# Performance work log

Hardware: AMD Instinct MI355X
Metric: run time of the kernel (lower is better)

## Reference

```python
import jax, jax.numpy as jnp
import numpy as np

WS = (4, 4, 4)          # window size (D, H, W)
DIM = 96
HEADS = 8
HEAD_DIM = DIM // HEADS
SCALE = HEAD_DIM ** (-0.5)
N = WS[0] * WS[1] * WS[2]  # 64 tokens per window


def _relative_position_index(ws):
    coords = np.stack(np.meshgrid(np.arange(ws[0]), np.arange(ws[1]), np.arange(ws[2]), indexing='ij'))
    cf = coords.reshape(3, -1)                       # [3, N]
    rel = cf[:, :, None] - cf[:, None, :]            # [3, N, N]
    rel = rel.transpose(1, 2, 0).astype(np.int64)    # [N, N, 3]
    rel[:, :, 0] += ws[0] - 1
    rel[:, :, 1] += ws[1] - 1
    rel[:, :, 2] += ws[2] - 1
    rel[:, :, 0] *= (2 * ws[1] - 1) * (2 * ws[2] - 1)
    rel[:, :, 1] *= 2 * ws[2] - 1
    return jnp.asarray(rel.sum(-1))                  # [N, N]

REL_IDX = _relative_position_index(WS)


def setup_inputs() -> dict:
    key = jax.random.key(0)
    ks = jax.random.split(key, 6)
    B = 4096   # total windows (64 images x 64 windows)
    nW = 64
    table_size = (2 * WS[0] - 1) * (2 * WS[1] - 1) * (2 * WS[2] - 1)  # 343
    return {
        'x': jax.random.normal(ks[0], (B, N, DIM), jnp.float32),
        'mask': jax.random.normal(ks[1], (nW, N, N), jnp.float32),
        'qkv_w': jax.random.normal(ks[2], (3 * DIM, DIM), jnp.float32) * 0.02,
        'proj_w': jax.random.normal(ks[3], (DIM, DIM), jnp.float32) * 0.02,
        'proj_b': jnp.zeros((DIM,), jnp.float32),
        'bias_table': jax.random.normal(ks[4], (table_size, HEADS), jnp.float32) * 0.02,
    }


def reference(x, mask, qkv_w, proj_w, proj_b, bias_table):
    B, n, C = x.shape
    # QKV projection (torch Linear: y = x @ W.T), split into heads
    qkv = (x @ qkv_w.T).reshape(B, n, 3, HEADS, HEAD_DIM)
    qkv = jnp.transpose(qkv, (2, 0, 3, 1, 4))        # [3, B, H, N, hd]
    q, k, v = qkv[0], qkv[1], qkv[2]
    attn = jnp.einsum('bhnd,bhmd->bhnm', q, k) * SCALE
    # gathered relative position bias: [N, N, H] -> [H, N, N]
    bias = bias_table[REL_IDX[:n, :n].reshape(-1)].reshape(n, n, HEADS)
    attn = attn + jnp.transpose(bias, (2, 0, 1))[None]
    # shifted-window mask add
    nW = mask.shape[0]
    attn = attn.reshape(B // nW, nW, HEADS, n, n) + mask[None, :, None]
    attn = attn.reshape(B, HEADS, n, n)
    attn = jax.nn.softmax(attn, axis=-1)
    out = jnp.einsum('bhnm,bhmd->bnhd', attn, v).reshape(B, n, C)
    return out @ proj_w.T + proj_b
```

## Files before the change

### kernel.cpp

```cpp
#include <hip/hip_runtime.h>
#include <stdint.h>


typedef float  f32x4  __attribute__((ext_vector_type(4)));
typedef float  f32x16 __attribute__((ext_vector_type(16)));
typedef short  short8 __attribute__((ext_vector_type(8)));

#define WS_WQKV_OFF  (8388608)
#define WS_WPROJ_OFF (8388608 + 55296)

__device__ __forceinline__ unsigned short f2bf(float f) {
  union { float f; uint32_t u; } v; v.f = f;
  uint32_t u = v.u + 0x7fffu + ((v.u >> 16) & 1u);
  return (unsigned short)(u >> 16);
}

__global__ void prep_weights(const float* __restrict__ qkv_w,
                             const float* __restrict__ proj_w,
                             unsigned short* __restrict__ ws16) {
  int tid = blockIdx.x * 256 + threadIdx.x;
  if (tid < 27648) {
    float v = qkv_w[tid];
    if (tid < 9216) v *= 0.28867513459481288f;
    ws16[WS_WQKV_OFF / 2 + tid] = f2bf(v);
  } else {
    int t = tid - 27648;
    ws16[WS_WPROJ_OFF / 2 + t] = f2bf(proj_w[t]);
  }
}

__global__ void prep_biasm(const float* __restrict__ mask,
                           const float* __restrict__ bias_table,
                           float* __restrict__ biasm) {
  int tid = blockIdx.x * 256 + threadIdx.x;
  int m = tid & 63;
  int r = (tid >> 6) & 63;
  int h = (tid >> 12) & 7;
  int w = tid >> 15;
  int dr = r >> 4, hr = (r >> 2) & 3, wr = r & 3;
  int dm = m >> 4, hm = (m >> 2) & 3, wm = m & 3;
  int idx = (dr - dm + 3) * 49 + (hr - hm + 3) * 7 + (wr - wm + 3);
  biasm[tid] = bias_table[idx * 8 + h] + mask[(w * 64 + r) * 64 + m];
}

__global__ __launch_bounds__(512, 4) void attn_main(
    const float* __restrict__ x, const float* __restrict__ proj_b,
    const unsigned short* __restrict__ ws16, const float* __restrict__ biasm,
    float* __restrict__ out) {
  __shared__ __align__(16) unsigned short xo[64][104];
  __shared__ __align__(16) unsigned short q_s[8][64][24];
  __shared__ __align__(16) unsigned short k_s[8][64][24];
  __shared__ __align__(16) unsigned short v_s[8][16][72];

  const int tid  = threadIdx.x;
  const int wv   = tid >> 6;
  const int lane = tid & 63;
  const int lo4 = lane & 15, hi4 = lane >> 4;
  const int lo5 = lane & 31, hi5 = lane >> 5;
  const int blk = blockIdx.x;
  const int wmask = blk & 63;

  const unsigned short* wqkv  = ws16 + WS_WQKV_OFF / 2;
  const unsigned short* wproj = ws16 + WS_WPROJ_OFF / 2;

  {
    int h = tid >> 6, r = tid & 63;
    *(uint2*)&q_s[h][r][12] = make_uint2(0u, 0u);
    *(uint2*)&k_s[h][r][12] = make_uint2(0u, 0u);
  }

  {
    const float4* xsrc = (const float4*)(x + (size_t)blk * (64 * 96));
    for (int i = tid; i < 1536; i += 512) {
      float4 v = xsrc[i];
      int t = i / 24, c4 = (i % 24) * 4;
      uint2 pk;
      pk.x = (uint32_t)f2bf(v.x) | ((uint32_t)f2bf(v.y) << 16);
      pk.y = (uint32_t)f2bf(v.z) | ((uint32_t)f2bf(v.w) << 16);
      *(uint2*)&xo[t][c4] = pk;
    }
  }
  __syncthreads();

  {
    const int mt = wv & 3;
    const int ng = wv >> 2;
    f32x4 acc[9];
#pragma unroll
    for (int nt = 0; nt < 9; ++nt) acc[nt] = (f32x4){0.f, 0.f, 0.f, 0.f};
    const int arow = mt * 16 + lo4;
#pragma unroll
    for (int ks = 0; ks < 3; ++ks) {
      short8 af = *(const short8*)&xo[arow][ks * 32 + hi4 * 8];
#pragma unroll
      for (int nt = 0; nt < 9; ++nt) {
        const int ntg = ng * 9 + nt;
        short8 bf = *(const short8*)&wqkv[(ntg * 16 + lo4) * 96 + ks * 32 + hi4 * 8];
        acc[nt] = __builtin_amdgcn_mfma_f32_16x16x32_bf16(af, bf, acc[nt], 0, 0, 0);
      }
    }
#pragma unroll
    for (int nt = 0; nt < 9; ++nt) {
      const int o = (ng * 9 + nt) * 16 + lo4;
      const int rem = o - (o >= 192 ? 192 : (o >= 96 ? 96 : 0));
      const int head = rem / 12;
      const int ch = rem - head * 12;
#pragma unroll
      for (int j = 0; j < 4; ++j) {
        const int r = mt * 16 + hi4 * 4 + j;
        unsigned short bv = f2bf(acc[nt][j]);
        if (o < 96)        q_s[head][r][ch] = bv;
        else if (o < 192)  k_s[head][r][ch] = bv;
        else               v_s[head][ch][r] = bv;
      }
    }
  }
  __syncthreads();

  {
    const int h = wv;
    const float* bm = biasm + (size_t)(wmask * 8 + h) * 4096;

    f32x16 c[2][2];
#pragma unroll
    for (int ti = 0; ti < 2; ++ti)
#pragma unroll
      for (int tj = 0; tj < 2; ++tj)
#pragma unroll
        for (int q4 = 0; q4 < 4; ++q4) {
          float4 b4 = *(const float4*)&bm[(tj * 32 + lo5) * 64 + ti * 32 + 8 * q4 + 4 * hi5];
          c[ti][tj][4 * q4 + 0] = b4.x;
          c[ti][tj][4 * q4 + 1] = b4.y;
          c[ti][tj][4 * q4 + 2] = b4.z;
          c[ti][tj][4 * q4 + 3] = b4.w;
        }
#pragma unroll
    for (int ti = 0; ti < 2; ++ti) {
      short8 af = *(const short8*)&k_s[h][ti * 32 + lo5][hi5 * 8];
#pragma unroll
      for (int tj = 0; tj < 2; ++tj) {
        short8 bf = *(const short8*)&q_s[h][tj * 32 + lo5][hi5 * 8];
        c[ti][tj] = __builtin_amdgcn_mfma_f32_32x32x16_bf16(af, bf, c[ti][tj], 0, 0, 0);
      }
    }

#pragma unroll
    for (int tj = 0; tj < 2; ++tj) {
      float mx = -1e30f;
#pragma unroll
      for (int ti = 0; ti < 2; ++ti)
#pragma unroll
        for (int reg = 0; reg < 16; ++reg) mx = fmaxf(mx, c[ti][tj][reg]);
      mx = fmaxf(mx, __shfl_xor(mx, 32));
      float sum = 0.f;
#pragma unroll
      for (int ti = 0; ti < 2; ++ti)
#pragma unroll
        for (int reg = 0; reg < 16; ++reg) {
          float e = __expf(c[ti][tj][reg] - mx);
          c[ti][tj][reg] = e;
          sum += e;
        }
      sum += __shfl_xor(sum, 32);
      float rs = 1.0f / sum;
#pragma unroll
      for (int ti = 0; ti < 2; ++ti)
#pragma unroll
        for (int reg = 0; reg < 16; ++reg) c[ti][tj][reg] *= rs;
    }

    uint32_t pk[2][2][8];
#pragma unroll
    for (int ti = 0; ti < 2; ++ti)
#pragma unroll
      for (int tj = 0; tj < 2; ++tj)
#pragma unroll
        for (int u = 0; u < 8; ++u)
          pk[ti][tj][u] = (uint32_t)f2bf(c[ti][tj][2 * u]) |
                          ((uint32_t)f2bf(c[ti][tj][2 * u + 1]) << 16);

    f32x16 oD[2];
    oD[0] = (f32x16)(0.f); oD[1] = (f32x16)(0.f);
#pragma unroll
    for (int kc = 0; kc < 4; ++kc) {
      const int ti = kc >> 1, base = 4 * (kc & 1);
      short8 av = *(const short8*)&v_s[h][lo5 & 15][kc * 16 + hi5 * 8];
#pragma unroll
      for (int tj = 0; tj < 2; ++tj) {
        uint32_t A0 = pk[ti][tj][base + 0], A1 = pk[ti][tj][base + 1];
        uint32_t A2 = pk[ti][tj][base + 2], A3 = pk[ti][tj][base + 3];
        uint32_t k0 = hi5 ? A2 : A0, k1 = hi5 ? A3 : A1;
        uint32_t s0 = (uint32_t)__shfl_xor((int)(hi5 ? A0 : A2), 32);
        uint32_t s1 = (uint32_t)__shfl_xor((int)(hi5 ? A1 : A3), 32);
        union { uint32_t u[4]; short8 s; } bfr;
        bfr.u[0] = hi5 ? s0 : k0;
        bfr.u[1] = hi5 ? s1 : k1;
        bfr.u[2] = hi5 ? k0 : s0;
        bfr.u[3] = hi5 ? k1 : s1;
        oD[tj] = __builtin_amdgcn_mfma_f32_32x32x16_bf16(av, bfr.s, oD[tj], 0, 0, 0);
      }
    }

#pragma unroll
    for (int tj = 0; tj < 2; ++tj) {
      const int q = tj * 32 + lo5;
#pragma unroll
      for (int reg = 0; reg < 8; ++reg) {
        const int q4 = reg >> 2, r2 = reg & 3;
        if (q4 == 0) {
          xo[q][h * 12 + r2 + 4 * hi5] = f2bf(oD[tj][reg]);
        } else if (hi5 == 0) {
          xo[q][h * 12 + 8 + r2] = f2bf(oD[tj][reg]);
        }
      }
    }
  }
  __syncthreads();

  {
    const int mt = wv >> 1;
    const int nb = (wv & 1) * 3;
    f32x4 acc[3];
#pragma unroll
    for (int nt = 0; nt < 3; ++nt) acc[nt] = (f32x4){0.f, 0.f, 0.f, 0.f};
    const int arow = mt * 16 + lo4;
#pragma unroll
    for (int ks = 0; ks < 3; ++ks) {
      short8 af = *(const short8*)&xo[arow][ks * 32 + hi4 * 8];
#pragma unroll
      for (int nt = 0; nt < 3; ++nt) {
        const int ntg = nb + nt;
        short8 bf = *(const short8*)&wproj[(ntg * 16 + lo4) * 96 + ks * 32 + hi4 * 8];
        acc[nt] = __builtin_amdgcn_mfma_f32_16x16x32_bf16(af, bf, acc[nt], 0, 0, 0);
      }
    }
    float* od = out + (size_t)blk * (64 * 96);
#pragma unroll
    for (int nt = 0; nt < 3; ++nt) {
      const int ntg = nb + nt;
      float pb = proj_b[ntg * 16 + lo4];
#pragma unroll
      for (int j = 0; j < 4; ++j)
        od[(mt * 16 + hi4 * 4 + j) * 96 + ntg * 16 + lo4] = acc[nt][j] + pb;
    }
  }
}

extern "C" void kernel_launch(void* const* d_in, const int* in_sizes, int n_in,
                              void* d_out, int out_size, void* d_ws, size_t ws_size,
                              hipStream_t stream) {
  const float* x          = (const float*)d_in[0];
  const float* mask       = (const float*)d_in[1];
  const float* qkv_w      = (const float*)d_in[2];
  const float* proj_w     = (const float*)d_in[3];
  const float* proj_b     = (const float*)d_in[4];
  const float* bias_table = (const float*)d_in[5];

  float* biasm = (float*)d_ws;
  unsigned short* ws16 = (unsigned short*)d_ws;

  prep_weights<<<144, 256, 0, stream>>>(qkv_w, proj_w, ws16);
  prep_biasm<<<8192, 256, 0, stream>>>(mask, bias_table, biasm);
  attn_main<<<4096, 512, 0, stream>>>(x, proj_b, ws16, biasm, (float*)d_out);
}
```

Baseline: 175.4 us.

## Transpose QKV MFMA for packed LDS stores, fold log2e, prefetch bias before barrier

After: 180.6 us. 1.03x slower.

```diff
diff --git a/kernel.cpp b/kernel.cpp
--- a/kernel.cpp
+++ b/kernel.cpp
@@ -1,4 +1,5 @@
 #include <hip/hip_runtime.h>
+#include <hip/hip_bf16.h>
 #include <stdint.h>
 
 
@@ -8,11 +9,15 @@
 
 #define WS_WQKV_OFF  (8388608)
 #define WS_WPROJ_OFF (8388608 + 55296)
+#define LOG2E 1.4426950408889634f
 
 __device__ __forceinline__ unsigned short f2bf(float f) {
-  union { float f; uint32_t u; } v; v.f = f;
-  uint32_t u = v.u + 0x7fffu + ((v.u >> 16) & 1u);
-  return (unsigned short)(u >> 16);
+  __hip_bfloat16 h = __float2bfloat16(f);
+  return *reinterpret_cast<unsigned short*>(&h);
+}
+__device__ __forceinline__ uint32_t pack2(float a, float b) {
+  __hip_bfloat162 h = __float22bfloat162_rn(float2{a, b});
+  return *reinterpret_cast<uint32_t*>(&h);
 }
 
 __global__ void prep_weights(const float* __restrict__ qkv_w,
@@ -21,7 +26,7 @@
   int tid = blockIdx.x * 256 + threadIdx.x;
   if (tid < 27648) {
     float v = qkv_w[tid];
-    if (tid < 9216) v *= 0.28867513459481288f;
+    if (tid < 9216) v *= (0.28867513459481288f * LOG2E);
     ws16[WS_WQKV_OFF / 2 + tid] = f2bf(v);
   } else {
     int t = tid - 27648;
@@ -40,7 +45,7 @@
   int dr = r >> 4, hr = (r >> 2) & 3, wr = r & 3;
   int dm = m >> 4, hm = (m >> 2) & 3, wm = m & 3;
   int idx = (dr - dm + 3) * 49 + (hr - hm + 3) * 7 + (wr - wm + 3);
-  biasm[tid] = bias_table[idx * 8 + h] + mask[(w * 64 + r) * 64 + m];
+  biasm[tid] = (bias_table[idx * 8 + h] + mask[(w * 64 + r) * 64 + m]) * LOG2E;
 }
 
 __global__ __launch_bounds__(512, 4) void attn_main(
@@ -74,54 +79,57 @@
     for (int i = tid; i < 1536; i += 512) {
       float4 v = xsrc[i];
       int t = i / 24, c4 = (i % 24) * 4;
-      uint2 pk;
-      pk.x = (uint32_t)f2bf(v.x) | ((uint32_t)f2bf(v.y) << 16);
-      pk.y = (uint32_t)f2bf(v.z) | ((uint32_t)f2bf(v.w) << 16);
-      *(uint2*)&xo[t][c4] = pk;
+      uint2 w2;
+      w2.x = pack2(v.x, v.y);
+      w2.y = pack2(v.z, v.w);
+      *(uint2*)&xo[t][c4] = w2;
     }
   }
   __syncthreads();
 
   {
-    const int mt = wv & 3;
-    const int ng = wv >> 2;
+    const int sub = wv & 3;
+    const int par = wv >> 2;
+    const int trow = sub * 16 + lo4;
     f32x4 acc[9];
 #pragma unroll
-    for (int nt = 0; nt < 9; ++nt) acc[nt] = (f32x4){0.f, 0.f, 0.f, 0.f};
-    const int arow = mt * 16 + lo4;
+    for (int i = 0; i < 9; ++i) acc[i] = (f32x4){0.f, 0.f, 0.f, 0.f};
 #pragma unroll
     for (int ks = 0; ks < 3; ++ks) {
-      short8 af = *(const short8*)&xo[arow][ks * 32 + hi4 * 8];
-#pragma unroll
-      for (int nt = 0; nt < 9; ++nt) {
-        const int ntg = ng * 9 + nt;
-        short8 bf = *(const short8*)&wqkv[(ntg * 16 + lo4) * 96 + ks * 32 + hi4 * 8];
-        acc[nt] = __builtin_amdgcn_mfma_f32_16x16x32_bf16(af, bf, acc[nt], 0, 0, 0);
-      }
-    }
-#pragma unroll
-    for (int nt = 0; nt < 9; ++nt) {
-      const int o = (ng * 9 + nt) * 16 + lo4;
-      const int rem = o - (o >= 192 ? 192 : (o >= 96 ? 96 : 0));
-      const int head = rem / 12;
-      const int ch = rem - head * 12;
-#pragma unroll
-      for (int j = 0; j < 4; ++j) {
-        const int r = mt * 16 + hi4 * 4 + j;
-        unsigned short bv = f2bf(acc[nt][j]);
-        if (o < 96)        q_s[head][r][ch] = bv;
-        else if (o < 192)  k_s[head][r][ch] = bv;
-        else               v_s[head][ch][r] = bv;
-      }
-    }
-  }
-  __syncthreads();
-
-  {
-    const int h = wv;
-    const float* bm = biasm + (size_t)(wmask * 8 + h) * 4096;
-
-    f32x16 c[2][2];
+      short8 bfX = *(const short8*)&xo[trow][ks * 32 + hi4 * 8];
+#pragma unroll
+      for (int i = 0; i < 9; ++i) {
+        const int mt = 2 * i + par;
+        short8 afW = *(const short8*)&wqkv[(mt * 16 + lo4) * 96 + ks * 32 + hi4 * 8];
+        acc[i] = __builtin_amdgcn_mfma_f32_16x16x32_bf16(afW, bfX, acc[i], 0, 0, 0);
+      }
+    }
+#pragma unroll
+    for (int i = 0; i < 9; ++i) {
+      const int mt = 2 * i + par;
+      const int o0 = mt * 16 + hi4 * 4;
+      if (o0 < 192) {
+        const int sec = (o0 >= 96) ? 96 : 0;
+        const int o = o0 - sec;
+        const int head = o / 12, ch = o - head * 12;
+        uint2 w2;
+        w2.x = pack2(acc[i][0], acc[i][1]);
+        w2.y = pack2(acc[i][2], acc[i][3]);
+        if (sec == 0) *(uint2*)&q_s[head][trow][ch] = w2;
+        else          *(uint2*)&k_s[head][trow][ch] = w2;
+      } else {
+        const int o = o0 - 192;
+        const int head = o / 12, ch = o - head * 12;
+#pragma unroll
+        for (int j = 0; j < 4; ++j)
+          v_s[head][ch + j][trow] = f2bf(acc[i][j]);
+      }
+    }
+  }
+
+  f32x16 c[2][2];
+  {
+    const float* bm = biasm + (size_t)(wmask * 8 + wv) * 4096;
 #pragma unroll
     for (int ti = 0; ti < 2; ++ti)
 #pragma unroll
@@ -134,6 +142,11 @@
           c[ti][tj][4 * q4 + 2] = b4.z;
           c[ti][tj][4 * q4 + 3] = b4.w;
         }
+  }
+  __syncthreads();
+
+  {
+    const int h = wv;
 #pragma unroll
     for (int ti = 0; ti < 2; ++ti) {
       short8 af = *(const short8*)&k_s[h][ti * 32 + lo5][hi5 * 8];
@@ -157,7 +170,7 @@
       for (int ti = 0; ti < 2; ++ti)
 #pragma unroll
         for (int reg = 0; reg < 16; ++reg) {
-          float e = __expf(c[ti][tj][reg] - mx);
+          float e = exp2f(c[ti][tj][reg] - mx);
           c[ti][tj][reg] = e;
           sum += e;
         }
@@ -169,15 +182,14 @@
         for (int reg = 0; reg < 16; ++reg) c[ti][tj][reg] *= rs;
     }
 
-    uint32_t pk[2][2][8];
+    uint32_t pkp[2][2][8];
 #pragma unroll
     for (int ti = 0; ti < 2; ++ti)
 #pragma unroll
       for (int tj = 0; tj < 2; ++tj)
 #pragma unroll
         for (int u = 0; u < 8; ++u)
-          pk[ti][tj][u] = (uint32_t)f2bf(c[ti][tj][2 * u]) |
-                          ((uint32_t)f2bf(c[ti][tj][2 * u + 1]) << 16);
+          pkp[ti][tj][u] = pack2(c[ti][tj][2 * u], c[ti][tj][2 * u + 1]);
 
     f32x16 oD[2];
     oD[0] = (f32x16)(0.f); oD[1] = (f32x16)(0.f);
@@ -187,8 +199,8 @@
       short8 av = *(const short8*)&v_s[h][lo5 & 15][kc * 16 + hi5 * 8];
 #pragma unroll
       for (int tj = 0; tj < 2; ++tj) {
-        uint32_t A0 = pk[ti][tj][base + 0], A1 = pk[ti][tj][base + 1];
-        uint32_t A2 = pk[ti][tj][base + 2], A3 = pk[ti][tj][base + 3];
+        uint32_t A0 = pkp[ti][tj][base + 0], A1 = pkp[ti][tj][base + 1];
+        uint32_t A2 = pkp[ti][tj][base + 2], A3 = pkp[ti][tj][base + 3];
         uint32_t k0 = hi5 ? A2 : A0, k1 = hi5 ? A3 : A1;
         uint32_t s0 = (uint32_t)__shfl_xor((int)(hi5 ? A0 : A2), 32);
         uint32_t s1 = (uint32_t)__shfl_xor((int)(hi5 ? A1 : A3), 32);
@@ -204,14 +216,15 @@
 #pragma unroll
     for (int tj = 0; tj < 2; ++tj) {
       const int q = tj * 32 + lo5;
-#pragma unroll
-      for (int reg = 0; reg < 8; ++reg) {
-        const int q4 = reg >> 2, r2 = reg & 3;
-        if (q4 == 0) {
-          xo[q][h * 12 + r2 + 4 * hi5] = f2bf(oD[tj][reg]);
-        } else if (hi5 == 0) {
-          xo[q][h * 12 + 8 + r2] = f2bf(oD[tj][reg]);
-        }
+      uint2 w2;
+      w2.x = pack2(oD[tj][0], oD[tj][1]);
+      w2.y = pack2(oD[tj][2], oD[tj][3]);
+      *(uint2*)&xo[q][h * 12 + 4 * hi5] = w2;
+      if (hi5 == 0) {
+        uint2 w3;
+        w3.x = pack2(oD[tj][4], oD[tj][5]);
+        w3.y = pack2(oD[tj][6], oD[tj][7]);
+        *(uint2*)&xo[q][h * 12 + 8] = w3;
       }
     }
   }
```
